# Performance work log

Measured on AMD Instinct MI355X. Metric: run time of the kernel, lower is better.

The kernel has to match this reference:

```python
import jax, jax.numpy as jnp
import numpy as np

COMMITMENT_COST = 0.25
EPSILON = 1e-5


def setup_inputs() -> dict:
    key = jax.random.key(0)
    k1, k2, k3 = jax.random.split(key, 3)
    B, T, D, M = 64, 512, 256, 400
    audio_semantic = jax.random.normal(k1, (B, T, D), dtype=jnp.float32)
    video_semantic = jax.random.normal(k2, (B, T, D), dtype=jnp.float32)
    # codebook initialized uniform in [-1/400, 1/400] as in the torch module
    init_bound = 1.0 / 400.0
    embedding = jax.random.uniform(k3, (M, D), dtype=jnp.float32,
                                   minval=-init_bound, maxval=init_bound)
    return {"audio_semantic": audio_semantic,
            "video_semantic": video_semantic,
            "embedding": embedding}


def _distances(x_flat, embedding, e_sq):
    x_sq = jnp.sum(x_flat * x_flat, axis=1, keepdims=True)
    return e_sq[None, :] + x_sq - 2.0 * (x_flat @ embedding.T)


def _perplexity(idx, M):
    n = idx.shape[0]
    avg_probs = jnp.bincount(idx, length=M).astype(jnp.float32) / n
    return jnp.exp(-jnp.sum(avg_probs * jnp.log(avg_probs + 1e-10)))


def _row_mode(idx_bt, M):
    # torch.mode returns the smallest most-frequent value; argmax of counts
    # returns the first (smallest) index on ties, which matches.
    counts = jax.vmap(lambda r: jnp.bincount(r, length=M))(idx_bt)  # [B, M]
    return jnp.argmax(counts, axis=-1)


def reference(audio_semantic, video_semantic, embedding):
    B, T, D = audio_semantic.shape
    M = embedding.shape[0]
    e_sq = jnp.sum(embedding * embedding, axis=1)  # [M]

    a_flat = audio_semantic.reshape(-1, D)
    v_flat = video_semantic.reshape(-1, D)

    # detached distances used for argmin / quantization
    a_d = _distances(jax.lax.stop_gradient(a_flat), embedding, e_sq)
    v_d = _distances(jax.lax.stop_gradient(v_flat), embedding, e_sq)

    # gradient-carrying distances for the contrastive term
    a_dg = _distances(a_flat, embedding, e_sq)
    v_dg = _distances(v_flat, embedding, e_sq)

    # softmax over codes of -sqrt(distance); clamp at 0 (distances are >= 0
    # mathematically, clamp only guards fp roundoff)
    a_ph = jax.nn.softmax(-jnp.sqrt(jnp.maximum(a_dg, 0.0)), axis=1)
    v_ph = jax.nn.softmax(-jnp.sqrt(jnp.maximum(v_dg, 0.0)), axis=1)
    a_pH = jnp.mean(a_ph.reshape(B, T, M), axis=1)  # [B, M]
    v_pH = jnp.mean(v_ph.reshape(B, T, M), axis=1)

    Scode = a_pH @ jnp.log(v_pH.T + 1e-10) + v_pH @ jnp.log(a_pH.T + 1e-10)
    MaxScode = jnp.max(-Scode)
    EScode = jnp.exp(Scode + MaxScode)
    EScode_sum = jnp.sum(EScode, axis=1)
    Lcmcm = -jnp.mean(jnp.log(jnp.diagonal(EScode) / (EScode_sum + EPSILON)))
    cmcm_loss = 0.5 * Lcmcm

    a_idx = jnp.argmin(a_d, axis=-1)  # [N]
    v_idx = jnp.argmin(v_d, axis=-1)
    a_quantized = embedding[a_idx].reshape(B, T, D)
    v_quantized = embedding[v_idx].reshape(B, T, D)

    # mode-agreement diagnostic
    a_mode = _row_mode(a_idx.reshape(B, T), M)
    v_mode = _row_mode(v_idx.reshape(B, T), M)
    equal_num = jnp.sum(a_mode == v_mode)

    sg = jax.lax.stop_gradient
    a_e = jnp.mean((audio_semantic - sg(a_quantized)) ** 2)
    av_e = jnp.mean((audio_semantic - sg(v_quantized)) ** 2)
    a_loss = COMMITMENT_COST * 2.0 * a_e + COMMITMENT_COST * av_e
    v_e = jnp.mean((video_semantic - sg(v_quantized)) ** 2)
    va_e = jnp.mean((video_semantic - sg(a_quantized)) ** 2)
    v_loss = COMMITMENT_COST * 2.0 * v_e + COMMITMENT_COST * va_e

    # straight-through estimator
    a_quantized = audio_semantic + sg(a_quantized - audio_semantic)
    v_quantized = video_semantic + sg(v_quantized - video_semantic)

    a_perplexity = _perplexity(a_idx, M)
    v_perplexity = _perplexity(v_idx, M)

    return (a_quantized, v_quantized, a_loss, v_loss,
            a_perplexity, v_perplexity, cmcm_loss, equal_num)
```

## Files before the change

kernel.cpp:

```cpp
#include <hip/hip_runtime.h>
#include <math.h>

#define NTOK 32768
#define DD 256
#define MM 400
#define BB 64
#define TT 512

#define WS_PH     0
#define WS_ROWCNT 204800
#define WS_ERR    409600
#define WS_ZERO_BYTES 410624
#define WS_IDX    410624
#define WS_ESQ    672768
#define WS_LG     674368
#define WS_SC     879168
#define WS_MODE   895552
#define WS_EH     896064
#define WS_EL     1100864

typedef __attribute__((ext_vector_type(8))) short bf16x8;
typedef __attribute__((ext_vector_type(4))) float f32x4;

__global__ void k_esq(const float* __restrict__ emb, float* __restrict__ esq,
                      unsigned short* __restrict__ eh, unsigned short* __restrict__ el) {
    int m = blockIdx.x, lane = threadIdx.x;
    float s = 0.f;
    for (int k = lane; k < DD; k += 64) {
        float e = emb[m * DD + k];
        s += e * e;
        unsigned u = __float_as_uint(e);
        unsigned short hu = (unsigned short)((u + 0x7FFFu + ((u >> 16) & 1u)) >> 16);
        float hf = __uint_as_float((unsigned)hu << 16);
        float lf = e - hf;
        unsigned ul = __float_as_uint(lf);
        unsigned short lu = (unsigned short)((ul + 0x7FFFu + ((ul >> 16) & 1u)) >> 16);
        eh[m * DD + k] = hu;
        el[m * DD + k] = lu;
    }
    #pragma unroll
    for (int off = 1; off < 64; off <<= 1) s += __shfl_xor(s, off, 64);
    if (lane == 0) esq[m] = s;
}

__launch_bounds__(256)
__global__ void k1_mfma(const float* __restrict__ a, const float* __restrict__ v,
                        const unsigned short* __restrict__ eh,
                        const unsigned short* __restrict__ el,
                        const float* __restrict__ esq_g,
                        float* __restrict__ pH_g,
                        int* __restrict__ rowcnt, int* __restrict__ idxws) {
    __shared__ __align__(16) unsigned short et[2][2][16 * 256];
    __shared__ float pH_w[4 * MM];
    __shared__ float xs_sh[4][16];

    const int tid = threadIdx.x;
    const int l   = tid & 63;
    const int wv  = tid >> 6;
    const int bx  = blockIdx.x;
    const int mod = bx >> 9;
    const int seg = bx & 511;
    const int blk0 = seg * 64;
    const int b    = seg >> 3;
    const int tok0 = blk0 + wv * 16;
    const float* xg = (mod == 0) ? a : v;

    const int r = l & 15;
    const int h = l >> 4;
    const int myTok = tok0 + r;
    const int rowoff = r << 8;
    const int sw3 = (r & 7) << 3;

    bf16x8 Xh[8], Xl[8];
    float xs_part = 0.f;
    #pragma unroll
    for (int s = 0; s < 8; ++s) {
        const float* p = xg + (size_t)myTok * DD + 32 * s + 8 * h;
        float4 f0 = *(const float4*)(p);
        float4 f1 = *(const float4*)(p + 4);
        bf16x8 th, tl;
        float e;
#define CVT(J, EV) { e = (EV); xs_part += e * e; \
        unsigned uu = __float_as_uint(e); \
        unsigned short hu = (unsigned short)((uu + 0x7FFFu + ((uu >> 16) & 1u)) >> 16); \
        float hf = __uint_as_float((unsigned)hu << 16); \
        float lf = e - hf; \
        unsigned ul = __float_as_uint(lf); \
        unsigned short lu = (unsigned short)((ul + 0x7FFFu + ((ul >> 16) & 1u)) >> 16); \
        th[J] = (short)hu; tl[J] = (short)lu; }
        CVT(0, f0.x) CVT(1, f0.y) CVT(2, f0.z) CVT(3, f0.w)
        CVT(4, f1.x) CVT(5, f1.y) CVT(6, f1.z) CVT(7, f1.w)
#undef CVT
        Xh[s] = th; Xl[s] = tl;
    }
    xs_part += __shfl_xor(xs_part, 16, 64);
    xs_part += __shfl_xor(xs_part, 32, 64);
    if (h == 0) xs_sh[wv][r] = xs_part;

#define STAGE(CT, BUF) { \
        for (int sg = wv; sg < 16; sg += 4) { \
            int hl = sg >> 3, s8 = sg & 7; \
            int u = (s8 << 6) + l; \
            int row_ = u >> 5, off16 = u & 31; \
            int colsh = (off16 << 3) ^ ((row_ & 7) << 3); \
            const unsigned short* gsrc = (hl ? el : eh) \
                + (size_t)((CT) * 16 + row_) * DD + colsh; \
            __builtin_amdgcn_global_load_lds( \
                (const __attribute__((address_space(1))) void*)gsrc, \
                (__attribute__((address_space(3))) void*)&et[BUF][hl][s8 << 9], \
                16, 0, 0); \
        } }

#define TILE_DOT(BUF, A0, A1, A2) { \
        const unsigned short* bh_ = &et[BUF][0][rowoff]; \
        const unsigned short* bl_ = &et[BUF][1][rowoff]; \
        _Pragma("unroll") \
        for (int s = 0; s < 8; ++s) { \
            int colsh = ((h << 3) + (s << 5)) ^ sw3; \
            bf16x8 Eh_ = *(const bf16x8*)&bh_[colsh]; \
            bf16x8 El_ = *(const bf16x8*)&bl_[colsh]; \
            A0 = __builtin_amdgcn_mfma_f32_16x16x32_bf16(Xh[s], Eh_, A0, 0, 0, 0); \
            A1 = __builtin_amdgcn_mfma_f32_16x16x32_bf16(Xh[s], El_, A1, 0, 0, 0); \
            A2 = __builtin_amdgcn_mfma_f32_16x16x32_bf16(Xl[s], Eh_, A2, 0, 0, 0); \
        } }

    STAGE(0, 0)
    float xs4[4], sqx4[4];

    float mind[4] = {1e30f, 1e30f, 1e30f, 1e30f};
    int   marg[4] = {0, 0, 0, 0};
    float se[4]   = {0.f, 0.f, 0.f, 0.f};
    for (int ct = 0; ct < 25; ++ct) {
        __syncthreads();
        if (ct == 0) {
            #pragma unroll
            for (int q = 0; q < 4; ++q) {
                xs4[q]  = xs_sh[wv][4 * h + q];
                sqx4[q] = sqrtf(xs4[q]);
            }
        }
        if (ct < 24) STAGE(ct + 1, (ct + 1) & 1)
        f32x4 a0 = {0.f,0.f,0.f,0.f}, a1 = {0.f,0.f,0.f,0.f}, a2 = {0.f,0.f,0.f,0.f};
        TILE_DOT(ct & 1, a0, a1, a2)
        const int c = ct * 16 + r;
        const float ec = esq_g[c];
        #pragma unroll
        for (int q = 0; q < 4; ++q) {
            float dot = a0[q] + a1[q] + a2[q];
            float dist = fmaf(-2.f, dot, xs4[q] + ec);
            float z = sqx4[q] - sqrtf(fmaxf(dist, 0.f));
            se[q] += __expf(z);
            if (dist < mind[q]) { mind[q] = dist; marg[q] = c; }
        }
    }
    #pragma unroll
    for (int q = 0; q < 4; ++q) {
        float bd = mind[q]; int bi = marg[q]; float s_ = se[q];
        #pragma unroll
        for (int off = 1; off < 16; off <<= 1) {
            float od = __shfl_xor(bd, off, 64);
            int   oi = __shfl_xor(bi, off, 64);
            s_ += __shfl_xor(s_, off, 64);
            if (od < bd || (od == bd && oi < bi)) { bd = od; bi = oi; }
        }
        se[q] = 1.f / s_;
        if (r == 0) {
            int n = tok0 + 4 * h + q;
            idxws[mod * NTOK + n] = bi;
            atomicAdd(&rowcnt[(mod * BB + b) * MM + bi], 1);
        }
    }

    __syncthreads();
    STAGE(0, 0)
    for (int ct = 0; ct < 25; ++ct) {
        __syncthreads();
        if (ct < 24) STAGE(ct + 1, (ct + 1) & 1)
        f32x4 a0 = {0.f,0.f,0.f,0.f}, a1 = {0.f,0.f,0.f,0.f}, a2 = {0.f,0.f,0.f,0.f};
        TILE_DOT(ct & 1, a0, a1, a2)
        const int c = ct * 16 + r;
        const float ec = esq_g[c];
        float val = 0.f;
        #pragma unroll
        for (int q = 0; q < 4; ++q) {
            float dot = a0[q] + a1[q] + a2[q];
            float dist = fmaf(-2.f, dot, xs4[q] + ec);
            float z = sqx4[q] - sqrtf(fmaxf(dist, 0.f));
            val = fmaf(__expf(z), se[q], val);
        }
        val += __shfl_xor(val, 16, 64);
        val += __shfl_xor(val, 32, 64);
        if (h == 0) pH_w[wv * MM + c] = val;
    }
#undef TILE_DOT
#undef STAGE

    __syncthreads();
    for (int m = tid; m < MM; m += 256) {
        float s = pH_w[m] + pH_w[MM + m] + pH_w[2 * MM + m] + pH_w[3 * MM + m];
        atomicAdd(&pH_g[(size_t)(mod * BB + b) * MM + m], s);
    }
}

__global__ void k_err(const float* __restrict__ a, const float* __restrict__ v,
                      const float* __restrict__ emb, const int* __restrict__ idxws,
                      float* __restrict__ out, float* __restrict__ err) {
    const int mod = blockIdx.y;
    const int tid = threadIdx.x;
    const int wv  = tid >> 6;
    const int d4  = (tid & 63) << 2;
    const float* x = (mod == 0) ? a : v;
    float* outm = out + (size_t)mod * NTOK * DD;

    float eo = 0.f, ec = 0.f;
    #pragma unroll
    for (int it = 0; it < 4; ++it) {
        const int n = blockIdx.x * 16 + (it << 2) + wv;
        const int ia = idxws[n];
        const int iv = idxws[NTOK + n];
        const int own = (mod == 0) ? ia : iv;
        const int oth = (mod == 0) ? iv : ia;

        float4 xv = *(const float4*)(x + (size_t)n * DD + d4);
        float4 qo = *(const float4*)(emb + (size_t)own * DD + d4);
        float4 qc = *(const float4*)(emb + (size_t)oth * DD + d4);
        f32x4 qv = {qo.x, qo.y, qo.z, qo.w};
        __builtin_nontemporal_store(qv, (f32x4*)(outm + (size_t)n * DD + d4));

        { float dx = xv.x - qo.x, dy = xv.y - qo.y, dz = xv.z - qo.z, dw = xv.w - qo.w;
          eo += dx * dx + dy * dy + dz * dz + dw * dw; }
        { float dx = xv.x - qc.x, dy = xv.y - qc.y, dz = xv.z - qc.z, dw = xv.w - qc.w;
          ec += dx * dx + dy * dy + dz * dz + dw * dw; }
    }

    #pragma unroll
    for (int off = 1; off < 64; off <<= 1) {
        eo += __shfl_xor(eo, off, 64);
        ec += __shfl_xor(ec, off, 64);
    }
    __shared__ float ro[4], rc[4];
    if ((tid & 63) == 0) { ro[wv] = eo; rc[wv] = ec; }
    __syncthreads();
    if (tid == 0) {
        int slot = blockIdx.x & 63;
        atomicAdd(&err[(mod * 2 + 0) * 64 + slot], ro[0] + ro[1] + ro[2] + ro[3]);
        atomicAdd(&err[(mod * 2 + 1) * 64 + slot], rc[0] + rc[1] + rc[2] + rc[3]);
    }
}

__global__ void k2_norm(float* __restrict__ pH, float* __restrict__ Lg) {
    int i = blockIdx.x * 256 + threadIdx.x;
    if (i < 2 * BB * MM) {
        float p = pH[i] * (1.f / TT);
        pH[i] = p;
        Lg[i] = logf(p + 1e-10f);
    }
}

__global__ void k3_mode(const int* __restrict__ rowcnt, int* __restrict__ modes) {
    int r = blockIdx.x, lane = threadIdx.x;
    const int* cnt = rowcnt + r * MM;
    int bc = -1, bi = 0x7fffffff;
    for (int m = lane; m < MM; m += 64) {
        int c = cnt[m];
        if (c > bc) { bc = c; bi = m; }
    }
    #pragma unroll
    for (int off = 1; off < 64; off <<= 1) {
        int oc = __shfl_xor(bc, off, 64);
        int oi = __shfl_xor(bi, off, 64);
        if (oc > bc || (oc == bc && oi < bi)) { bc = oc; bi = oi; }
    }
    if (lane == 0) modes[r] = bi;
}

__global__ void k4_scode(const float* __restrict__ pH, const float* __restrict__ Lg,
                         float* __restrict__ Sc) {
    int i = blockIdx.x;
    int tid = threadIdx.x, lane = tid & 63, wv = tid >> 6;
    const float* aPH = pH + (size_t)i * MM;
    const float* vPH = pH + (size_t)(BB + i) * MM;
    for (int jj = 0; jj < 16; ++jj) {
        int j = wv * 16 + jj;
        const float* Lv = Lg + (size_t)(BB + j) * MM;
        const float* La = Lg + (size_t)j * MM;
        float s = 0.f;
        for (int m = lane; m < MM; m += 64)
            s += aPH[m] * Lv[m] + vPH[m] * La[m];
        #pragma unroll
        for (int off = 1; off < 64; off <<= 1) s += __shfl_xor(s, off, 64);
        if (lane == 0) Sc[i * BB + j] = s;
    }
}

__global__ void k5_final(const float* __restrict__ Sc, const int* __restrict__ rowcnt,
                         const float* __restrict__ err, const int* __restrict__ modes,
                         float* __restrict__ outs) {
    __shared__ float red[4];
    __shared__ float mx_sh;
    int tid = threadIdx.x;
    int lane = tid & 63, wv = tid >> 6;

    float lmin = 1e30f;
    for (int i = tid; i < BB * BB; i += 256) lmin = fminf(lmin, Sc[i]);
    #pragma unroll
    for (int off = 1; off < 64; off <<= 1) lmin = fminf(lmin, __shfl_xor(lmin, off, 64));
    if (lane == 0) red[wv] = lmin;
    __syncthreads();
    if (tid == 0) mx_sh = -fminf(fminf(red[0], red[1]), fminf(red[2], red[3]));
    __syncthreads();
    float Mx = mx_sh;

    if (wv == 0) {
        int i = lane;
        float rs = 0.f;
        for (int j = 0; j < BB; ++j) rs += __expf(Sc[i * BB + j] + Mx);
        float dg = __expf(Sc[i * BB + i] + Mx);
        float term = logf(dg / (rs + 1e-5f));
        #pragma unroll
        for (int off = 1; off < 64; off <<= 1) term += __shfl_xor(term, off, 64);
        if (lane == 0) outs[4] = 0.5f * (-(term / (float)BB));
    } else if (wv == 1 || wv == 2) {
        int mod = wv - 1;
        float s = 0.f;
        for (int m = lane; m < MM; m += 64) {
            int c = 0;
            for (int bb = 0; bb < BB; ++bb)
                c += rowcnt[(size_t)(mod * BB + bb) * MM + m];
            float p = (float)c * (1.f / (float)NTOK);
            s += p * logf(p + 1e-10f);
        }
        #pragma unroll
        for (int off = 1; off < 64; off <<= 1) s += __shfl_xor(s, off, 64);
        if (lane == 0) outs[2 + mod] = __expf(-s);
    } else {
        float e0 = err[0 * 64 + lane], e1 = err[1 * 64 + lane];
        float e2 = err[2 * 64 + lane], e3 = err[3 * 64 + lane];
        int eq = (modes[lane] == modes[BB + lane]) ? 1 : 0;
        #pragma unroll
        for (int off = 1; off < 64; off <<= 1) {
            e0 += __shfl_xor(e0, off, 64);
            e1 += __shfl_xor(e1, off, 64);
            e2 += __shfl_xor(e2, off, 64);
            e3 += __shfl_xor(e3, off, 64);
            eq += __shfl_xor(eq, off, 64);
        }
        if (lane == 0) {
            outs[5] = (float)eq;
            const float inv = 1.f / (float)((size_t)NTOK * DD);
            float a_e = e0 * inv, av_e = e1 * inv;
            float v_e = e2 * inv, va_e = e3 * inv;
            outs[0] = 0.5f * a_e + 0.25f * av_e;
            outs[1] = 0.5f * v_e + 0.25f * va_e;
        }
    }
}

extern "C" void kernel_launch(void* const* d_in, const int* in_sizes, int n_in,
                              void* d_out, int out_size, void* d_ws, size_t ws_size,
                              hipStream_t stream) {
    (void)in_sizes; (void)n_in; (void)out_size; (void)ws_size;
    const float* a   = (const float*)d_in[0];
    const float* v   = (const float*)d_in[1];
    const float* emb = (const float*)d_in[2];
    float* out = (float*)d_out;
    char* ws = (char*)d_ws;

    float* pH_g   = (float*)(ws + WS_PH);
    int*   rowcnt = (int*)(ws + WS_ROWCNT);
    float* err    = (float*)(ws + WS_ERR);
    int*   idxws  = (int*)(ws + WS_IDX);
    float* esq    = (float*)(ws + WS_ESQ);
    float* Lg     = (float*)(ws + WS_LG);
    float* Sc     = (float*)(ws + WS_SC);
    int*   modes  = (int*)(ws + WS_MODE);
    unsigned short* eh = (unsigned short*)(ws + WS_EH);
    unsigned short* el = (unsigned short*)(ws + WS_EL);

    hipMemsetAsync(d_ws, 0, WS_ZERO_BYTES, stream);
    k_esq<<<MM, 64, 0, stream>>>(emb, esq, eh, el);
    k1_mfma<<<1024, 256, 0, stream>>>(a, v, eh, el, esq, pH_g, rowcnt, idxws);
    k_err<<<dim3(2048, 2), 256, 0, stream>>>(a, v, emb, idxws, out, err);
    k2_norm<<<200, 256, 0, stream>>>(pH_g, Lg);
    k3_mode<<<128, 64, 0, stream>>>(rowcnt, modes);
    k4_scode<<<BB, 256, 0, stream>>>(pH_g, Lg, Sc);
    k5_final<<<1, 256, 0, stream>>>(Sc, rowcnt, err, modes, out + (size_t)2 * NTOK * DD);
}
```

Measured before the change: 340.5 us.

## Drop low-part X MFMA and cache softmax logits in fp16 registers

Removes the third bf16 split product (X low times E high), which lowers the precision of the distance dot product. Logits z from the first pass are kept in fp16 registers, so the second pass no longer re-stages the codebook or recomputes the MFMA distances. This roughly halves the matrix work and cuts the second round of LDS staging and barriers. In exchange it raises register pressure (50 half2 values per thread) and adds precision risk to the argmin and the softmax.

```diff
diff --git a/kernel.cpp b/kernel.cpp
--- a/kernel.cpp
+++ b/kernel.cpp
@@ -1,4 +1,5 @@
 #include <hip/hip_runtime.h>
+#include <hip/hip_fp16.h>
 #include <math.h>
 
 #define NTOK 32768
@@ -71,27 +72,22 @@
     const int rowoff = r << 8;
     const int sw3 = (r & 7) << 3;
 
-    bf16x8 Xh[8], Xl[8];
+    bf16x8 Xh[8];
     float xs_part = 0.f;
     #pragma unroll
     for (int s = 0; s < 8; ++s) {
         const float* p = xg + (size_t)myTok * DD + 32 * s + 8 * h;
         float4 f0 = *(const float4*)(p);
         float4 f1 = *(const float4*)(p + 4);
-        bf16x8 th, tl;
+        bf16x8 th;
         float e;
 #define CVT(J, EV) { e = (EV); xs_part += e * e; \
         unsigned uu = __float_as_uint(e); \
-        unsigned short hu = (unsigned short)((uu + 0x7FFFu + ((uu >> 16) & 1u)) >> 16); \
-        float hf = __uint_as_float((unsigned)hu << 16); \
-        float lf = e - hf; \
-        unsigned ul = __float_as_uint(lf); \
-        unsigned short lu = (unsigned short)((ul + 0x7FFFu + ((ul >> 16) & 1u)) >> 16); \
-        th[J] = (short)hu; tl[J] = (short)lu; }
+        th[J] = (short)(unsigned short)((uu + 0x7FFFu + ((uu >> 16) & 1u)) >> 16); }
         CVT(0, f0.x) CVT(1, f0.y) CVT(2, f0.z) CVT(3, f0.w)
         CVT(4, f1.x) CVT(5, f1.y) CVT(6, f1.z) CVT(7, f1.w)
 #undef CVT
-        Xh[s] = th; Xl[s] = tl;
+        Xh[s] = th;
     }
     xs_part += __shfl_xor(xs_part, 16, 64);
     xs_part += __shfl_xor(xs_part, 32, 64);
@@ -111,7 +107,7 @@
                 16, 0, 0); \
         } }
 
-#define TILE_DOT(BUF, A0, A1, A2) { \
+#define TILE_DOT(BUF, A0, A1) { \
         const unsigned short* bh_ = &et[BUF][0][rowoff]; \
         const unsigned short* bl_ = &et[BUF][1][rowoff]; \
         _Pragma("unroll") \
@@ -121,7 +117,6 @@
             bf16x8 El_ = *(const bf16x8*)&bl_[colsh]; \
             A0 = __builtin_amdgcn_mfma_f32_16x16x32_bf16(Xh[s], Eh_, A0, 0, 0, 0); \
             A1 = __builtin_amdgcn_mfma_f32_16x16x32_bf16(Xh[s], El_, A1, 0, 0, 0); \
-            A2 = __builtin_amdgcn_mfma_f32_16x16x32_bf16(Xl[s], Eh_, A2, 0, 0, 0); \
         } }
 
     STAGE(0, 0)
@@ -130,6 +125,8 @@
     float mind[4] = {1e30f, 1e30f, 1e30f, 1e30f};
     int   marg[4] = {0, 0, 0, 0};
     float se[4]   = {0.f, 0.f, 0.f, 0.f};
+    __half2 zst[25][2];
+    #pragma unroll
     for (int ct = 0; ct < 25; ++ct) {
         __syncthreads();
         if (ct == 0) {
@@ -140,18 +137,22 @@
             }
         }
         if (ct < 24) STAGE(ct + 1, (ct + 1) & 1)
-        f32x4 a0 = {0.f,0.f,0.f,0.f}, a1 = {0.f,0.f,0.f,0.f}, a2 = {0.f,0.f,0.f,0.f};
-        TILE_DOT(ct & 1, a0, a1, a2)
+        f32x4 a0 = {0.f,0.f,0.f,0.f}, a1 = {0.f,0.f,0.f,0.f};
+        TILE_DOT(ct & 1, a0, a1)
         const int c = ct * 16 + r;
         const float ec = esq_g[c];
+        float z4[4];
         #pragma unroll
         for (int q = 0; q < 4; ++q) {
-            float dot = a0[q] + a1[q] + a2[q];
+            float dot = a0[q] + a1[q];
             float dist = fmaf(-2.f, dot, xs4[q] + ec);
             float z = sqx4[q] - sqrtf(fmaxf(dist, 0.f));
+            z4[q] = z;
             se[q] += __expf(z);
             if (dist < mind[q]) { mind[q] = dist; marg[q] = c; }
         }
+        zst[ct][0] = __floats2half2_rn(z4[0], z4[1]);
+        zst[ct][1] = __floats2half2_rn(z4[2], z4[3]);
     }
     #pragma unroll
     for (int q = 0; q < 4; ++q) {
@@ -171,23 +172,13 @@
         }
     }
 
-    __syncthreads();
-    STAGE(0, 0)
+    #pragma unroll
     for (int ct = 0; ct < 25; ++ct) {
-        __syncthreads();
-        if (ct < 24) STAGE(ct + 1, (ct + 1) & 1)
-        f32x4 a0 = {0.f,0.f,0.f,0.f}, a1 = {0.f,0.f,0.f,0.f}, a2 = {0.f,0.f,0.f,0.f};
-        TILE_DOT(ct & 1, a0, a1, a2)
         const int c = ct * 16 + r;
-        const float ec = esq_g[c];
-        float val = 0.f;
-        #pragma unroll
-        for (int q = 0; q < 4; ++q) {
-            float dot = a0[q] + a1[q] + a2[q];
-            float dist = fmaf(-2.f, dot, xs4[q] + ec);
-            float z = sqx4[q] - sqrtf(fmaxf(dist, 0.f));
-            val = fmaf(__expf(z), se[q], val);
-        }
+        float val = __expf(__low2float(zst[ct][0]))  * se[0]
+                  + __expf(__high2float(zst[ct][0])) * se[1]
+                  + __expf(__low2float(zst[ct][1]))  * se[2]
+                  + __expf(__high2float(zst[ct][1])) * se[3];
         val += __shfl_xor(val, 16, 64);
         val += __shfl_xor(val, 32, 64);
         if (h == 0) pH_w[wv * MM + c] = val;
```

After: 327.9 us. 3.7% less time.
